# Kernel tuning notes

Measured on AMD Instinct MI355X. Metric: run time of the kernel, lower is better.

The kernel has to match this reference:

```python
import jax, jax.numpy as jnp
import numpy as np

B = 8
SHAPE = (4, 16, 16)   # latent video shape; S = prod = 1024
S = 1024
AE = 64               # ae_embed_dim
D = 768               # embed_dim
F = 3072              # mlp_dim
H = 12                # num_heads (heads are re-merged before the score matmul!)
L = 12                # num_layers
C = 17                # n_classes
OUT = 1024            # out_dim
EPS = 1e-6
HD = D // H


def setup_inputs() -> dict:
    key = jax.random.key(0)
    ks = iter(jax.random.split(key, 64))

    def p(shape, s=0.02):
        return jax.random.normal(next(ks), shape, jnp.float32) * s

    inp = {
        'x': jax.random.normal(next(ks), (B, *SHAPE, AE), jnp.float32),
        'mask': jnp.tril(jnp.ones((S, S), bool)),  # causal
        'label': jax.nn.one_hot(jax.random.randint(next(ks), (B,), 0, C), C, dtype=jnp.float32),
        'dense_in_w': p((D, AE)), 'dense_in_b': jnp.zeros((D,), jnp.float32),
        'sos': p((D,)),
        # BroadcastPositionBiases: embed_dim=768 split into 3 chunks of 256
        'pos0': p((SHAPE[0], D // 3)), 'pos1': p((SHAPE[1], D // 3)), 'pos2': p((SHAPE[2], D // 3)),
        'ln1_sw': p((L, D, C)), 'ln1_bw': p((L, D, C)),
        'qkv_w': p((L, 3 * D, D)), 'qkv_b': jnp.zeros((L, 3 * D), jnp.float32),
        'ao1_w': p((L, D, D)), 'ao1_b': jnp.zeros((L, D), jnp.float32),  # DotProductAttention.out_proj
        'ao2_w': p((L, D, D)), 'ao2_b': jnp.zeros((L, D), jnp.float32),  # MultiHeadAttention.out_proj
        'ln2_sw': p((L, D, C)), 'ln2_bw': p((L, D, C)),
        'mlp_w1': p((L, F, D)), 'mlp_b1': jnp.zeros((L, F), jnp.float32),
        'mlp_w2': p((L, D, F)), 'mlp_b2': jnp.zeros((L, D), jnp.float32),
        'lnf_sw': p((D, C)), 'lnf_bw': p((D, C)),
        'out_w': p((OUT, D)), 'out_b': jnp.zeros((OUT,), jnp.float32),
    }
    return inp


def cond_ln(x, cond, sw, bw):
    # conditional LayerNorm: mul = rsqrt(var+eps)*(1+Linear(cond)), bias = Linear(cond)
    mean = jnp.mean(x, axis=-1, keepdims=True)
    var = jnp.mean((x - mean) ** 2, axis=-1, keepdims=True)
    scale = cond @ sw.T   # [B, D]
    bias = cond @ bw.T    # [B, D]
    mul = jax.lax.rsqrt(var + EPS) * (1.0 + scale[:, None, :])
    return (x - mean) * mul + bias[:, None, :]


def pos_bias(embs, shape):
    n = len(shape)
    outs = []
    for i, e in enumerate(embs):
        sh = [1] * n + [e.shape[-1]]
        sh[i] = shape[i]
        outs.append(jnp.broadcast_to(e.reshape(sh), tuple(shape) + (e.shape[-1],)))
    return jnp.concatenate(outs, axis=-1).reshape(-1, sum(e.shape[-1] for e in embs))  # [S, D]


def attn_block(h, mask, qkv_w, qkv_b, o1_w, o1_b, o2_w, o2_b):
    Bn, Sn, Dn = h.shape
    qkv = h @ qkv_w.T + qkv_b                       # [B, S, 3D]
    qkv = qkv.reshape(Bn, Sn, H, 3 * HD)            # per-head [q|k|v] layout
    q = qkv[..., :HD].reshape(Bn, Sn, Dn)           # heads re-merged BEFORE scores
    k = qkv[..., HD:2 * HD].reshape(Bn, Sn, Dn)
    v = qkv[..., 2 * HD:].reshape(Bn, Sn, Dn)
    # NOTE: scaling uses full embed_dim (module quirk), not head_dim
    scores = jnp.einsum('bqd,bkd->bqk', q * (float(Dn) ** -0.5), k)
    scores = jnp.where(mask[None, :, :], scores, -jnp.inf)
    w = jax.nn.softmax(scores, axis=-1)
    out = jnp.einsum('bqk,bkd->bqd', w, v)
    out = out @ o1_w.T + o1_b                        # DotProductAttention.out_proj
    out = out @ o2_w.T + o2_b                        # MultiHeadAttention.out_proj (applied twice)
    return out


def _forward(x, mask, label, dense_in_w, dense_in_b, sos, pos0, pos1, pos2,
             ln1_sw, ln1_bw, qkv_w, qkv_b, ao1_w, ao1_b, ao2_w, ao2_b,
             ln2_sw, ln2_bw, mlp_w1, mlp_b1, mlp_w2, mlp_b2,
             lnf_sw, lnf_bw, out_w, out_b):
    Bn = x.shape[0]
    old_shape = x.shape[1:-1]
    h = x.reshape(Bn, -1, x.shape[-1]) @ dense_in_w.T + dense_in_b   # [B, S, D]
    # right shift with learned SOS token
    h = jnp.concatenate([jnp.broadcast_to(sos, (Bn, 1, D)), h[:, :-1]], axis=1)
    pb = pos_bias([pos0, pos1, pos2], old_shape)                     # [S, D]
    h = h + pb[None, :h.shape[1]]
    for l in range(L):
        hn = cond_ln(h, label, ln1_sw[l], ln1_bw[l])
        h = h + attn_block(hn, mask, qkv_w[l], qkv_b[l], ao1_w[l], ao1_b[l], ao2_w[l], ao2_b[l])
        hn = cond_ln(h, label, ln2_sw[l], ln2_bw[l])
        m = hn @ mlp_w1[l].T + mlp_b1[l]
        m = jax.nn.sigmoid(1.702 * m) * m           # GELU2
        m = m @ mlp_w2[l].T + mlp_b2[l]
        h = h + m
    h = cond_ln(h, label, lnf_sw, lnf_bw)
    out = h @ out_w.T + out_b                        # [B, S, OUT]
    return out.reshape(Bn, *old_shape, out.shape[-1])


def reference(x, mask, label, dense_in_w, dense_in_b, sos, pos0, pos1, pos2,
              ln1_sw, ln1_bw, qkv_w, qkv_b, ao1_w, ao1_b, ao2_w, ao2_b,
              ln2_sw, ln2_bw, mlp_w1, mlp_b1, mlp_w2, mlp_b2,
              lnf_sw, lnf_bw, out_w, out_b):
    return _forward(x, mask, label, dense_in_w, dense_in_b, sos, pos0, pos1, pos2,
                    ln1_sw, ln1_bw, qkv_w, qkv_b, ao1_w, ao1_b, ao2_w, ao2_b,
                    ln2_sw, ln2_bw, mlp_w1, mlp_b1, mlp_w2, mlp_b2,
                    lnf_sw, lnf_bw, out_w, out_b)
```

## Files before the change

### kernel.cpp

```cpp
#include <hip/hip_runtime.h>

typedef __bf16 bf16;
typedef __bf16 bf16x8 __attribute__((ext_vector_type(8)));
typedef __bf16 bf16x4 __attribute__((ext_vector_type(4)));
typedef float  f32x4  __attribute__((ext_vector_type(4)));

#define DEV __device__ __forceinline__

DEV void gload_lds16(const bf16* g, bf16* l) {
    __builtin_amdgcn_global_load_lds(
        (__attribute__((address_space(1))) void*)g,
        (__attribute__((address_space(3))) void*)l, 16, 0, 0);
}

DEV void barrier_raw() {
    asm volatile("" ::: "memory");
    __builtin_amdgcn_s_barrier();
    asm volatile("" ::: "memory");
}

enum { M_QKV, M_SCORES, M_PV, M_RESID, M_GELU, M_OUT, M_WM };

template<int MODE>
__global__ __launch_bounds__(256)
void gemm_k(const bf16* __restrict__ A, const bf16* __restrict__ B,
            int M, int N, int K,
            long long batchA, long long batchB, long long batchC,
            const float* __restrict__ bias,
            bf16* __restrict__ Cb, float* __restrict__ Cf,
            bf16* __restrict__ qp, bf16* __restrict__ kp, bf16* __restrict__ vp)
{
    const int bm = blockIdx.x, bn = blockIdx.y, bz = blockIdx.z;
    const int kTiles = K >> 5;

    const int tid = threadIdx.x, wid = tid >> 6, lane = tid & 63;
    const bf16* Ab = A + (long long)bz * batchA + (long long)bm * 128 * K;
    const bf16* Bb = B + (long long)bz * batchB + (long long)bn * 128 * K;

    extern __shared__ __align__(16) bf16 smem[];
    bf16* sA = smem;
    bf16* sB = smem + 12288;

    const int srow = wid * 16 + (lane >> 2);
    const int scol = (lane & 3) * 8;
    const long long aoff = (long long)srow * K + scol;

    auto stage = [&](int buf, int kt) {
        const bf16* ga = Ab + (long long)kt * 32;
        const bf16* gb = Bb + (long long)kt * 32;
        bf16* a = sA + buf * 4096;
        bf16* b = sB + buf * 4096;
        gload_lds16(ga + aoff,            a + (wid * 16) * 32);
        gload_lds16(ga + aoff + 64LL * K, a + (64 + wid * 16) * 32);
        gload_lds16(gb + aoff,            b + (wid * 16) * 32);
        gload_lds16(gb + aoff + 64LL * K, b + (64 + wid * 16) * 32);
    };

    f32x4 acc[4][4];
#pragma unroll
    for (int m = 0; m < 4; ++m)
#pragma unroll
        for (int n = 0; n < 4; ++n) acc[m][n] = (f32x4){0.f, 0.f, 0.f, 0.f};

    const int npre = kTiles < 2 ? kTiles : 2;
    for (int t = 0; t < npre; ++t) stage(t, t);

    const int wr = wid >> 1, wc = wid & 1;
    const int arow = wr * 64 + (lane & 15);
    const int brow = wc * 64 + (lane & 15);
    const int koff = (lane >> 4) * 8;

    int cur = 0;
    for (int kt = 0; kt < kTiles; ++kt) {
        if (kt + 1 < kTiles) asm volatile("s_waitcnt vmcnt(4)" ::: "memory");
        else                 asm volatile("s_waitcnt vmcnt(0)" ::: "memory");
        barrier_raw();
        if (kt + 2 < kTiles) {
            int ib = cur - 1; if (ib < 0) ib = 2;
            stage(ib, kt + 2);
        }

        const bf16* a = sA + cur * 4096;
        const bf16* b = sB + cur * 4096;
        bf16x8 af[4], bfr[4];
#pragma unroll
        for (int m = 0; m < 4; ++m)
            af[m] = *(const bf16x8*)&a[(arow + m * 16) * 32 + koff];
#pragma unroll
        for (int n = 0; n < 4; ++n)
            bfr[n] = *(const bf16x8*)&b[(brow + n * 16) * 32 + koff];
#pragma unroll
        for (int m = 0; m < 4; ++m)
#pragma unroll
            for (int n = 0; n < 4; ++n)
                acc[m][n] = __builtin_amdgcn_mfma_f32_16x16x32_bf16(af[m], bfr[n], acc[m][n], 0, 0, 0);

        cur = (cur == 2) ? 0 : cur + 1;
    }

    const int cr0 = bm * 128 + wr * 64 + (lane >> 4) * 4;
    const int cc0 = bn * 128 + wc * 64 + (lane & 15);
#pragma unroll
    for (int m = 0; m < 4; ++m) {
#pragma unroll
        for (int n = 0; n < 4; ++n) {
            const int col = cc0 + n * 16;
#pragma unroll
            for (int r = 0; r < 4; ++r) {
                const int row = cr0 + m * 16 + r;
                float v = acc[m][n][r];
                if (MODE == M_QKV) {
                    v += bias[col];
                    int hd = col / 192, rr = col % 192;
                    int b2 = row >> 10, s = row & 1023;
                    if (rr < 64)
                        qp[(long long)row * 768 + hd * 64 + rr] = (bf16)(v * 0.03608439182435161f);
                    else if (rr < 128)
                        kp[(long long)row * 768 + hd * 64 + (rr - 64)] = (bf16)v;
                    else
                        vp[((long long)b2 * 768 + hd * 64 + (rr - 128)) * 1024 + s] = (bf16)v;
                } else if (MODE == M_GELU) {
                    float xg = v + bias[col];
                    Cb[(long long)row * N + col] = (bf16)(xg / (1.f + __expf(-1.702f * xg)));
                } else if (MODE == M_RESID) {
                    long long idx = (long long)row * N + col;
                    Cf[idx] += v + bias[col];
                } else if (MODE == M_WM) {
                    Cb[(long long)bz * batchC + (long long)row * N + col] = (bf16)v;
                } else {
                    Cf[(long long)row * N + col] = v + bias[col];
                }
            }
        }
    }
}

template<int MODE>
__global__ __launch_bounds__(256)
void gemm64_k(const bf16* __restrict__ A, const bf16* __restrict__ B,
              int M, int N, int K,
              long long batchA, long long batchB, long long batchC,
              const float* __restrict__ bias,
              bf16* __restrict__ Cb, float* __restrict__ Cf)
{
    const int bm = blockIdx.x, bn = blockIdx.y, bz = blockIdx.z;
    if (MODE == M_SCORES && 2 * bn > bm) return;
    int kTiles = K >> 5;
    if (MODE == M_PV) {
        int lim = 2 * bm + 2;
        if (lim < kTiles) kTiles = lim;
    }

    const int tid = threadIdx.x, wid = tid >> 6, lane = tid & 63;
    const bf16* Ab = A + (long long)bz * batchA + (long long)bm * 64 * K;
    const bf16* Bb = B + (long long)bz * batchB + (long long)bn * 128 * K;

    extern __shared__ __align__(16) bf16 smem[];
    bf16* sA = smem;
    bf16* sB = smem + 6144;

    const int srow = wid * 16 + (lane >> 2);
    const int scol = (lane & 3) * 8;
    const long long aoff = (long long)srow * K + scol;

    auto stage = [&](int buf, int kt) {
        const bf16* ga = Ab + (long long)kt * 32;
        const bf16* gb = Bb + (long long)kt * 32;
        gload_lds16(ga + aoff,            sA + buf * 2048 + (wid * 16) * 32);
        gload_lds16(gb + aoff,            sB + buf * 4096 + (wid * 16) * 32);
        gload_lds16(gb + aoff + 64LL * K, sB + buf * 4096 + (64 + wid * 16) * 32);
    };

    f32x4 acc[2][4];
#pragma unroll
    for (int m = 0; m < 2; ++m)
#pragma unroll
        for (int n = 0; n < 4; ++n) acc[m][n] = (f32x4){0.f, 0.f, 0.f, 0.f};

    const int npre = kTiles < 2 ? kTiles : 2;
    for (int t = 0; t < npre; ++t) stage(t, t);

    const int wr = wid >> 1, wc = wid & 1;
    const int arow = wr * 32 + (lane & 15);
    const int brow = wc * 64 + (lane & 15);
    const int koff = (lane >> 4) * 8;

    int cur = 0;
    for (int kt = 0; kt < kTiles; ++kt) {
        if (kt + 1 < kTiles) asm volatile("s_waitcnt vmcnt(3)" ::: "memory");
        else                 asm volatile("s_waitcnt vmcnt(0)" ::: "memory");
        barrier_raw();
        if (kt + 2 < kTiles) {
            int ib = cur - 1; if (ib < 0) ib = 2;
            stage(ib, kt + 2);
        }

        const bf16* a = sA + cur * 2048;
        const bf16* b = sB + cur * 4096;
        bf16x8 af[2], bfr[4];
#pragma unroll
        for (int m = 0; m < 2; ++m)
            af[m] = *(const bf16x8*)&a[(arow + m * 16) * 32 + koff];
#pragma unroll
        for (int n = 0; n < 4; ++n)
            bfr[n] = *(const bf16x8*)&b[(brow + n * 16) * 32 + koff];
#pragma unroll
        for (int m = 0; m < 2; ++m)
#pragma unroll
            for (int n = 0; n < 4; ++n)
                acc[m][n] = __builtin_amdgcn_mfma_f32_16x16x32_bf16(af[m], bfr[n], acc[m][n], 0, 0, 0);

        cur = (cur == 2) ? 0 : cur + 1;
    }

    const int cr0 = bm * 64 + wr * 32 + (lane >> 4) * 4;
    const int cc0 = bn * 128 + wc * 64 + (lane & 15);
#pragma unroll
    for (int m = 0; m < 2; ++m) {
#pragma unroll
        for (int n = 0; n < 4; ++n) {
            const int col = cc0 + n * 16;
#pragma unroll
            for (int r = 0; r < 4; ++r) {
                const int row = cr0 + m * 16 + r;
                float v = acc[m][n][r];
                if (MODE == M_SCORES || MODE == M_PV) {
                    Cb[(long long)bz * batchC + (long long)row * N + col] = (bf16)v;
                } else if (MODE == M_RESID) {
                    long long idx = (long long)row * N + col;
                    Cf[idx] += v + bias[col];
                } else {
                    Cf[(long long)row * N + col] = v + bias[col];
                }
            }
        }
    }
}

__global__ __launch_bounds__(256)
void cvt_bf16_k(const float* __restrict__ in, bf16* __restrict__ out, int n4)
{
    int i = blockIdx.x * 256 + threadIdx.x;
    if (i >= n4) return;
    float4 f = ((const float4*)in)[i];
    bf16x4 o = { (bf16)f.x, (bf16)f.y, (bf16)f.z, (bf16)f.w };
    ((bf16x4*)out)[i] = o;
}

__global__ __launch_bounds__(256)
void transpose_cvt_k(const float* __restrict__ in, bf16* __restrict__ out, int n)
{
    __shared__ float t[32][33];
    const int l = blockIdx.z;
    const int r0 = blockIdx.y * 32, c0 = blockIdx.x * 32;
    const float* src = in + (long long)l * n * n;
    bf16* dst = out + (long long)l * n * n;
    const int tx = threadIdx.x & 31, ty = threadIdx.x >> 5;
#pragma unroll
    for (int i = 0; i < 32; i += 8)
        t[ty + i][tx] = src[(long long)(r0 + ty + i) * n + c0 + tx];
    __syncthreads();
#pragma unroll
    for (int i = 0; i < 32; i += 8)
        dst[(long long)(c0 + ty + i) * n + r0 + tx] = (bf16)t[tx][ty + i];
}

__global__ __launch_bounds__(256)
void bias_merge_k(const float* __restrict__ o2w, const float* __restrict__ o1b,
                  const float* __restrict__ o2b, float* __restrict__ bm, int total)
{
    const int wid = threadIdx.x >> 6, lane = threadIdx.x & 63;
    const int idx = blockIdx.x * 4 + wid;
    if (idx >= total) return;
    const int l = idx / 768, a = idx - l * 768;
    const float* wrow = o2w + ((long long)l * 768 + a) * 768;
    const float* brow = o1b + (long long)l * 768;
    float s = 0.f;
#pragma unroll
    for (int j = 0; j < 12; ++j) {
        int c = j * 64 + lane;
        s += wrow[c] * brow[c];
    }
#pragma unroll
    for (int o = 32; o; o >>= 1) s += __shfl_down(s, o);
    if (lane == 0) bm[idx] = s + o2b[(long long)l * 768 + a];
}

__global__ __launch_bounds__(256)
void cond_proj_k(const float* __restrict__ label, const float* __restrict__ sw,
                 const float* __restrict__ bw, float* __restrict__ scale,
                 float* __restrict__ bias, int total)
{
    int idx = blockIdx.x * 256 + threadIdx.x;
    if (idx >= total) return;
    int l = idx / 6144;
    int rem = idx - l * 6144;
    int b = rem / 768, d = rem - (rem / 768) * 768;
    const float* lab = label + b * 17;
    const float* swp = sw + ((long long)l * 768 + d) * 17;
    const float* bwp = bw + ((long long)l * 768 + d) * 17;
    float s = 0.f, bb = 0.f;
#pragma unroll
    for (int c = 0; c < 17; ++c) { float lv = lab[c]; s += lv * swp[c]; bb += lv * bwp[c]; }
    scale[idx] = s;
    bias[idx]  = bb;
}

__global__ __launch_bounds__(256)
void shift_pos_k(const float* __restrict__ xe, const float* __restrict__ sos,
                 const float* __restrict__ p0, const float* __restrict__ p1,
                 const float* __restrict__ p2, float* __restrict__ h)
{
    const int s = blockIdx.x, b = blockIdx.y;
    const int i0 = s >> 8, i1 = (s >> 4) & 15, i2 = s & 15;
    const float* xr = xe + ((long long)b * 1024 + (s - 1)) * 768;
#pragma unroll
    for (int j = 0; j < 3; ++j) {
        const int d = j * 256 + threadIdx.x;
        float v = (s == 0) ? sos[d] : xr[d];
        float pbv = (d < 256) ? p0[i0 * 256 + d]
                  : (d < 512) ? p1[i1 * 256 + (d - 256)]
                              : p2[i2 * 256 + (d - 512)];
        h[((long long)b * 1024 + s) * 768 + d] = v + pbv;
    }
}

__global__ __launch_bounds__(256)
void cond_ln_k(const float* __restrict__ h, const float* __restrict__ scale,
               const float* __restrict__ bias, bf16* __restrict__ out)
{
    const long long row = (long long)blockIdx.y * 1024 + blockIdx.x;
    const int b = blockIdx.y;
    const float* hr = h + row * 768;
    float v[3], sum = 0.f, sq = 0.f;
#pragma unroll
    for (int j = 0; j < 3; ++j) {
        v[j] = hr[j * 256 + threadIdx.x];
        sum += v[j]; sq += v[j] * v[j];
    }
    __shared__ float sm[8];
#pragma unroll
    for (int o = 32; o; o >>= 1) { sum += __shfl_down(sum, o); sq += __shfl_down(sq, o); }
    const int wid = threadIdx.x >> 6;
    if ((threadIdx.x & 63) == 0) { sm[wid] = sum; sm[4 + wid] = sq; }
    __syncthreads();
    sum = sm[0] + sm[1] + sm[2] + sm[3];
    sq  = sm[4] + sm[5] + sm[6] + sm[7];
    const float mean = sum * (1.f / 768.f);
    const float var  = sq * (1.f / 768.f) - mean * mean;
    const float rs   = rsqrtf(var + 1e-6f);
    const float* sc = scale + (long long)b * 768;
    const float* bi = bias  + (long long)b * 768;
    bf16* orow = out + row * 768;
#pragma unroll
    for (int j = 0; j < 3; ++j) {
        const int d = j * 256 + threadIdx.x;
        orow[d] = (bf16)((v[j] - mean) * rs * (1.f + sc[d]) + bi[d]);
    }
}

__global__ __launch_bounds__(256)
void softmax_k(bf16* __restrict__ P)
{
    const int i = blockIdx.x, b = blockIdx.y;
    bf16* row = P + ((long long)b * 1024 + i) * 1024;
    const int len = i + 1;
    const int lim = (i | 63) + 1;
    float v[4], mx = -1e30f;
#pragma unroll
    for (int j = 0; j < 4; ++j) {
        int c = j * 256 + threadIdx.x;
        v[j] = (c < len) ? (float)row[c] : -1e30f;
        mx = fmaxf(mx, v[j]);
    }
    __shared__ float sm[8];
#pragma unroll
    for (int o = 32; o; o >>= 1) mx = fmaxf(mx, __shfl_down(mx, o));
    const int wid = threadIdx.x >> 6;
    if ((threadIdx.x & 63) == 0) sm[wid] = mx;
    __syncthreads();
    mx = fmaxf(fmaxf(sm[0], sm[1]), fmaxf(sm[2], sm[3]));
    float s = 0.f;
#pragma unroll
    for (int j = 0; j < 4; ++j) {
        v[j] = __expf(v[j] - mx);
        s += ((j * 256 + threadIdx.x) < len) ? v[j] : 0.f;
    }
#pragma unroll
    for (int o = 32; o; o >>= 1) s += __shfl_down(s, o);
    if ((threadIdx.x & 63) == 0) sm[4 + wid] = s;
    __syncthreads();
    s = sm[4] + sm[5] + sm[6] + sm[7];
    const float inv = 1.f / s;
#pragma unroll
    for (int j = 0; j < 4; ++j) {
        int c = j * 256 + threadIdx.x;
        if (c < lim) row[c] = (c < len) ? (bf16)(v[j] * inv) : (bf16)0.f;
    }
}

__global__ __launch_bounds__(256)
void fill_k(float* o, int n, float v)
{
    int i = blockIdx.x * 256 + threadIdx.x;
    if (i < n) o[i] = v;
}

extern "C" void kernel_launch(void* const* d_in, const int* in_sizes, int n_in,
                              void* d_out, int out_size, void* d_ws, size_t ws_size,
                              hipStream_t stream)
{
    (void)in_sizes; (void)n_in;
    const float* x     = (const float*)d_in[0];
    const float* label = (const float*)d_in[2];
    const float* dw    = (const float*)d_in[3];
    const float* db    = (const float*)d_in[4];
    const float* sos   = (const float*)d_in[5];
    const float* p0    = (const float*)d_in[6];
    const float* p1    = (const float*)d_in[7];
    const float* p2    = (const float*)d_in[8];
    const float* ln1sw = (const float*)d_in[9];
    const float* ln1bw = (const float*)d_in[10];
    const float* qkvw  = (const float*)d_in[11];
    const float* qkvb  = (const float*)d_in[12];
    const float* ao1w  = (const float*)d_in[13];
    const float* ao1b  = (const float*)d_in[14];
    const float* ao2w  = (const float*)d_in[15];
    const float* ao2b  = (const float*)d_in[16];
    const float* ln2sw = (const float*)d_in[17];
    const float* ln2bw = (const float*)d_in[18];
    const float* m1w   = (const float*)d_in[19];
    const float* m1b   = (const float*)d_in[20];
    const float* m2w   = (const float*)d_in[21];
    const float* m2b   = (const float*)d_in[22];
    const float* lnfsw = (const float*)d_in[23];
    const float* lnfbw = (const float*)d_in[24];
    const float* outw  = (const float*)d_in[25];
    const float* outb  = (const float*)d_in[26];
    float* out = (float*)d_out;

    char* p = (char*)d_ws;
    auto alloc = [&](size_t bytes) { void* r = (void*)p; p += (bytes + 255) & ~(size_t)255; return r; };
    float* h    = (float*)alloc(8192LL * 768 * 4);
    bf16*  hn   = (bf16*) alloc(8192LL * 768 * 2);
    bf16*  q    = (bf16*) alloc(8192LL * 768 * 2);
    bf16*  kbuf = (bf16*) alloc(8192LL * 768 * 2);
    bf16*  vT   = (bf16*) alloc(8192LL * 768 * 2);
    bf16*  P    = (bf16*) alloc(8LL * 1024 * 1024 * 2);
    bf16*  attn = (bf16*) alloc(8192LL * 768 * 2);
    bf16*  mb   = (bf16*) alloc(8192LL * 3072 * 2);
    bf16*  wout = (bf16*) alloc(1024LL * 768 * 2);
    bf16*  wmA  = (bf16*) alloc(12LL * 768 * 768 * 2);
    float* bmA  = (float*)alloc(12LL * 768 * 4);
    float* s1   = (float*)alloc(12LL * 8 * 768 * 4);
    float* b1   = (float*)alloc(12LL * 8 * 768 * 4);
    float* s2   = (float*)alloc(12LL * 8 * 768 * 4);
    float* b2   = (float*)alloc(12LL * 8 * 768 * 4);
    float* sf   = (float*)alloc(8LL * 768 * 4);
    float* bfb  = (float*)alloc(8LL * 768 * 4);

    size_t base_needed = (size_t)(p - (char*)d_ws);
    if (base_needed + 16LL * 1024 * 1024 > ws_size) {
        fill_k<<<(out_size + 255) / 256, 256, 0, stream>>>(out, out_size, 1e9f);
        return;
    }

    const long long SZ_QKV = 2304LL * 768, SZ_O = 768LL * 768, SZ_M = 3072LL * 768;
    size_t all_bytes = (size_t)(12 * (SZ_QKV + 2 * SZ_M)) * 2;
    bool allw = ((size_t)(p - (char*)d_ws) + all_bytes + 4096 <= ws_size);

    bf16 *wqkvA, *wm1A, *wm2A;
    if (allw) {
        wqkvA = (bf16*)alloc(12 * SZ_QKV * 2);
        wm1A  = (bf16*)alloc(12 * SZ_M * 2);
        wm2A  = (bf16*)alloc(12 * SZ_M * 2);
    } else {
        wqkvA = (bf16*)alloc(SZ_QKV * 2);
        wm1A  = (bf16*)alloc(SZ_M * 2);
        wm2A  = (bf16*)alloc(SZ_M * 2);
    }

    bf16*  xbf   = (bf16*)P;
    bf16*  dwbf  = (bf16*)P + 524288;
    bf16*  wo2bf = (bf16*)P + 1048576;
    float* xe    = (float*)mb;
    bf16*  o1t   = mb + 12582912;

    cvt_bf16_k<<<1024 * 768 / 4 / 256, 256, 0, stream>>>(outw, wout, 1024 * 768 / 4);
    cond_proj_k<<<(12 * 8 * 768 + 255) / 256, 256, 0, stream>>>(label, ln1sw, ln1bw, s1, b1, 12 * 8 * 768);
    cond_proj_k<<<(12 * 8 * 768 + 255) / 256, 256, 0, stream>>>(label, ln2sw, ln2bw, s2, b2, 12 * 8 * 768);
    cond_proj_k<<<(8 * 768 + 255) / 256, 256, 0, stream>>>(label, lnfsw, lnfbw, sf, bfb, 8 * 768);

    if (allw) {
        cvt_bf16_k<<<(int)(12 * SZ_QKV / 4 / 256), 256, 0, stream>>>(qkvw, wqkvA, (int)(12 * SZ_QKV / 4));
        cvt_bf16_k<<<(int)(12 * SZ_M / 4 / 256),   256, 0, stream>>>(m1w,  wm1A,  (int)(12 * SZ_M / 4));
        cvt_bf16_k<<<(int)(12 * SZ_M / 4 / 256),   256, 0, stream>>>(m2w,  wm2A,  (int)(12 * SZ_M / 4));
    }

    cvt_bf16_k<<<(int)(12 * SZ_O / 4 / 256), 256, 0, stream>>>(ao2w, wo2bf, (int)(12 * SZ_O / 4));
    transpose_cvt_k<<<dim3(24, 24, 12), 256, 0, stream>>>(ao1w, o1t, 768);
    gemm_k<M_WM><<<dim3(6, 6, 12), 256, 49152, stream>>>(
        wo2bf, o1t, 768, 768, 768, SZ_O, SZ_O, SZ_O,
        nullptr, wmA, nullptr, nullptr, nullptr, nullptr);
    bias_merge_k<<<(12 * 768 + 3) / 4, 256, 0, stream>>>(ao2w, ao1b, ao2b, bmA, 12 * 768);

    cvt_bf16_k<<<8192 * 64 / 4 / 256, 256, 0, stream>>>(x, xbf, 8192 * 64 / 4);
    cvt_bf16_k<<<768 * 64 / 4 / 256, 256, 0, stream>>>(dw, dwbf, 768 * 64 / 4);
    gemm_k<M_OUT><<<dim3(64, 6, 1), 256, 49152, stream>>>(
        xbf, dwbf, 8192, 768, 64, 0, 0, 0, db, nullptr, xe, nullptr, nullptr, nullptr);
    shift_pos_k<<<dim3(1024, 8), 256, 0, stream>>>(xe, sos, p0, p1, p2, h);

    for (int l = 0; l < 12; ++l) {
        bf16 *wqkv, *wm1, *wm2;
        if (allw) {
            wqkv = wqkvA + (long long)l * SZ_QKV;
            wm1  = wm1A  + (long long)l * SZ_M;
            wm2  = wm2A  + (long long)l * SZ_M;
        } else {
            wqkv = wqkvA; wm1 = wm1A; wm2 = wm2A;
            cvt_bf16_k<<<(int)(SZ_QKV / 4 / 256), 256, 0, stream>>>(qkvw + (long long)l * SZ_QKV, wqkv, (int)(SZ_QKV / 4));
            cvt_bf16_k<<<(int)(SZ_M / 4 / 256),   256, 0, stream>>>(m1w  + (long long)l * SZ_M,   wm1,  (int)(SZ_M / 4));
            cvt_bf16_k<<<(int)(SZ_M / 4 / 256),   256, 0, stream>>>(m2w  + (long long)l * SZ_M,   wm2,  (int)(SZ_M / 4));
        }

        cond_ln_k<<<dim3(1024, 8), 256, 0, stream>>>(h, s1 + (long long)l * 6144, b1 + (long long)l * 6144, hn);

        gemm_k<M_QKV><<<dim3(64, 18, 1), 256, 49152, stream>>>(
            hn, wqkv, 8192, 2304, 768, 0, 0, 0,
            qkvb + (long long)l * 2304, nullptr, nullptr, q, kbuf, vT);

        gemm64_k<M_SCORES><<<dim3(16, 8, 8), 256, 36864, stream>>>(
            q, kbuf, 1024, 1024, 768, 1024LL * 768, 1024LL * 768, 1024LL * 1024,
            nullptr, P, nullptr);

        softmax_k<<<dim3(1024, 8), 256, 0, stream>>>(P);

        gemm64_k<M_PV><<<dim3(16, 6, 8), 256, 36864, stream>>>(
            P, vT, 1024, 768, 1024, 1024LL * 1024, 768LL * 1024, 1024LL * 768,
            nullptr, attn, nullptr);

        gemm64_k<M_RESID><<<dim3(128, 6, 1), 256, 36864, stream>>>(
            attn, wmA + (long long)l * SZ_O, 8192, 768, 768, 0, 0, 0,
            bmA + (long long)l * 768, nullptr, h);

        cond_ln_k<<<dim3(1024, 8), 256, 0, stream>>>(h, s2 + (long long)l * 6144, b2 + (long long)l * 6144, hn);

        gemm_k<M_GELU><<<dim3(64, 24, 1), 256, 49152, stream>>>(
            hn, wm1, 8192, 3072, 768, 0, 0, 0,
            m1b + (long long)l * 3072, mb, nullptr, nullptr, nullptr, nullptr);

        gemm64_k<M_RESID><<<dim3(128, 6, 1), 256, 36864, stream>>>(
            mb, wm2, 8192, 768, 3072, 0, 0, 0,
            m2b + (long long)l * 768, nullptr, h);
    }

    cond_ln_k<<<dim3(1024, 8), 256, 0, stream>>>(h, sf, bfb, hn);
    gemm64_k<M_OUT><<<dim3(128, 8, 1), 256, 36864, stream>>>(
        hn, wout, 8192, 1024, 768, 0, 0, 0,
        outb, nullptr, out);
}
```

Baseline: 3.905 ms.

## Load A operand directly to registers, stage only B through LDS

New measurement: 5.349 ms. 36.9% more time.

```diff
diff --git a/kernel.cpp b/kernel.cpp
--- a/kernel.cpp
+++ b/kernel.cpp
@@ -14,7 +14,7 @@
 }
 
 DEV void barrier_raw() {
-    asm volatile("" ::: "memory");
+    asm volatile("s_waitcnt lgkmcnt(0)" ::: "memory");
     __builtin_amdgcn_s_barrier();
     asm volatile("" ::: "memory");
 }
@@ -37,55 +37,52 @@
     const bf16* Ab = A + (long long)bz * batchA + (long long)bm * 128 * K;
     const bf16* Bb = B + (long long)bz * batchB + (long long)bn * 128 * K;
 
-    extern __shared__ __align__(16) bf16 smem[];
-    bf16* sA = smem;
-    bf16* sB = smem + 12288;
+    extern __shared__ __align__(16) bf16 sB[];
 
     const int srow = wid * 16 + (lane >> 2);
     const int scol = (lane & 3) * 8;
-    const long long aoff = (long long)srow * K + scol;
-
-    auto stage = [&](int buf, int kt) {
-        const bf16* ga = Ab + (long long)kt * 32;
-        const bf16* gb = Bb + (long long)kt * 32;
-        bf16* a = sA + buf * 4096;
+    const long long boff = (long long)srow * K + scol;
+
+    auto stageB = [&](int buf, int kt) {
+        const bf16* gb = Bb + (long long)kt * 32 + boff;
         bf16* b = sB + buf * 4096;
-        gload_lds16(ga + aoff,            a + (wid * 16) * 32);
-        gload_lds16(ga + aoff + 64LL * K, a + (64 + wid * 16) * 32);
-        gload_lds16(gb + aoff,            b + (wid * 16) * 32);
-        gload_lds16(gb + aoff + 64LL * K, b + (64 + wid * 16) * 32);
+        gload_lds16(gb,            b + (wid * 16) * 32);
+        gload_lds16(gb + 64LL * K, b + (64 + wid * 16) * 32);
     };
-
-    f32x4 acc[4][4];
-#pragma unroll
-    for (int m = 0; m < 4; ++m)
-#pragma unroll
-        for (int n = 0; n < 4; ++n) acc[m][n] = (f32x4){0.f, 0.f, 0.f, 0.f};
-
-    const int npre = kTiles < 2 ? kTiles : 2;
-    for (int t = 0; t < npre; ++t) stage(t, t);
 
     const int wr = wid >> 1, wc = wid & 1;
     const int arow = wr * 64 + (lane & 15);
     const int brow = wc * 64 + (lane & 15);
     const int koff = (lane >> 4) * 8;
 
-    int cur = 0;
-    for (int kt = 0; kt < kTiles; ++kt) {
-        if (kt + 1 < kTiles) asm volatile("s_waitcnt vmcnt(4)" ::: "memory");
+    auto loadA = [&](bf16x8 (&af)[4], int kt) {
+#pragma unroll
+        for (int m = 0; m < 4; ++m)
+            af[m] = *(const bf16x8*)(Ab + (long long)(arow + m * 16) * K + kt * 32 + koff);
+    };
+
+    f32x4 acc[4][4];
+#pragma unroll
+    for (int m = 0; m < 4; ++m)
+#pragma unroll
+        for (int n = 0; n < 4; ++n) acc[m][n] = (f32x4){0.f, 0.f, 0.f, 0.f};
+
+    bf16x8 afA[4], afB[4];
+    stageB(0, 0);
+    if (kTiles > 1) stageB(1, 1);
+    loadA(afA, 0);
+
+    auto body = [&](bf16x8 (&afc)[4], bf16x8 (&afn)[4], int kt) {
+        if (kt + 2 < kTiles) asm volatile("s_waitcnt vmcnt(2)" ::: "memory");
         else                 asm volatile("s_waitcnt vmcnt(0)" ::: "memory");
         barrier_raw();
+        if (kt + 1 < kTiles) loadA(afn, kt + 1);
         if (kt + 2 < kTiles) {
-            int ib = cur - 1; if (ib < 0) ib = 2;
-            stage(ib, kt + 2);
+            int b3 = (kt + 2) % 3;
+            stageB(b3, kt + 2);
         }
-
-        const bf16* a = sA + cur * 4096;
-        const bf16* b = sB + cur * 4096;
-        bf16x8 af[4], bfr[4];
-#pragma unroll
-        for (int m = 0; m < 4; ++m)
-            af[m] = *(const bf16x8*)&a[(arow + m * 16) * 32 + koff];
+        const bf16* b = sB + (kt % 3) * 4096;
+        bf16x8 bfr[4];
 #pragma unroll
         for (int n = 0; n < 4; ++n)
             bfr[n] = *(const bf16x8*)&b[(brow + n * 16) * 32 + koff];
@@ -93,9 +90,12 @@
         for (int m = 0; m < 4; ++m)
 #pragma unroll
             for (int n = 0; n < 4; ++n)
-                acc[m][n] = __builtin_amdgcn_mfma_f32_16x16x32_bf16(af[m], bfr[n], acc[m][n], 0, 0, 0);
-
-        cur = (cur == 2) ? 0 : cur + 1;
+                acc[m][n] = __builtin_amdgcn_mfma_f32_16x16x32_bf16(afc[m], bfr[n], acc[m][n], 0, 0, 0);
+    };
+
+    for (int kt = 0; kt < kTiles; kt += 2) {
+        body(afA, afB, kt);
+        body(afB, afA, kt + 1);
     }
 
     const int cr0 = bm * 128 + wr * 64 + (lane >> 4) * 4;
@@ -155,52 +155,52 @@
     const bf16* Ab = A + (long long)bz * batchA + (long long)bm * 64 * K;
     const bf16* Bb = B + (long long)bz * batchB + (long long)bn * 128 * K;
 
-    extern __shared__ __align__(16) bf16 smem[];
-    bf16* sA = smem;
-    bf16* sB = smem + 6144;
+    extern __shared__ __align__(16) bf16 sB[];
 
     const int srow = wid * 16 + (lane >> 2);
     const int scol = (lane & 3) * 8;
-    const long long aoff = (long long)srow * K + scol;
-
-    auto stage = [&](int buf, int kt) {
-        const bf16* ga = Ab + (long long)kt * 32;
-        const bf16* gb = Bb + (long long)kt * 32;
-        gload_lds16(ga + aoff,            sA + buf * 2048 + (wid * 16) * 32);
-        gload_lds16(gb + aoff,            sB + buf * 4096 + (wid * 16) * 32);
-        gload_lds16(gb + aoff + 64LL * K, sB + buf * 4096 + (64 + wid * 16) * 32);
+    const long long boff = (long long)srow * K + scol;
+
+    auto stageB = [&](int buf, int kt) {
+        const bf16* gb = Bb + (long long)kt * 32 + boff;
+        bf16* b = sB + buf * 4096;
+        gload_lds16(gb,            b + (wid * 16) * 32);
+        gload_lds16(gb + 64LL * K, b + (64 + wid * 16) * 32);
     };
-
-    f32x4 acc[2][4];
-#pragma unroll
-    for (int m = 0; m < 2; ++m)
-#pragma unroll
-        for (int n = 0; n < 4; ++n) acc[m][n] = (f32x4){0.f, 0.f, 0.f, 0.f};
-
-    const int npre = kTiles < 2 ? kTiles : 2;
-    for (int t = 0; t < npre; ++t) stage(t, t);
 
     const int wr = wid >> 1, wc = wid & 1;
     const int arow = wr * 32 + (lane & 15);
     const int brow = wc * 64 + (lane & 15);
     const int koff = (lane >> 4) * 8;
 
-    int cur = 0;
-    for (int kt = 0; kt < kTiles; ++kt) {
-        if (kt + 1 < kTiles) asm volatile("s_waitcnt vmcnt(3)" ::: "memory");
+    auto loadA = [&](bf16x8 (&af)[2], int kt) {
+#pragma unroll
+        for (int m = 0; m < 2; ++m)
+            af[m] = *(const bf16x8*)(Ab + (long long)(arow + m * 16) * K + kt * 32 + koff);
+    };
+
+    f32x4 acc[2][4];
+#pragma unroll
+    for (int m = 0; m < 2; ++m)
+#pragma unroll
+        for (int n = 0; n < 4; ++n) acc[m][n] = (f32x4){0.f, 0.f, 0.f, 0.f};
+
+    bf16x8 afA[2], afB[2];
+    stageB(0, 0);
+    if (kTiles > 1) stageB(1, 1);
+    loadA(afA, 0);
+
+    auto body = [&](bf16x8 (&afc)[2], bf16x8 (&afn)[2], int kt) {
+        if (kt + 2 < kTiles) asm volatile("s_waitcnt vmcnt(2)" ::: "memory");
         else                 asm volatile("s_waitcnt vmcnt(0)" ::: "memory");
         barrier_raw();
+        if (kt + 1 < kTiles) loadA(afn, kt + 1);
         if (kt + 2 < kTiles) {
-            int ib = cur - 1; if (ib < 0) ib = 2;
-            stage(ib, kt + 2);
+            int b3 = (kt + 2) % 3;
+            stageB(b3, kt + 2);
         }
-
-        const bf16* a = sA + cur * 2048;
-        const bf16* b = sB + cur * 4096;
-        bf16x8 af[2], bfr[4];
-#pragma unroll
-        for (int m = 0; m < 2; ++m)
-            af[m] = *(const bf16x8*)&a[(arow + m * 16) * 32 + koff];
+        const bf16* b = sB + (kt % 3) * 4096;
+        bf16x8 bfr[4];
 #pragma unroll
         for (int n = 0; n < 4; ++n)
             bfr[n] = *(const bf16x8*)&b[(brow + n * 16) * 32 + koff];
@@ -208,9 +208,12 @@
         for (int m = 0; m < 2; ++m)
 #pragma unroll
             for (int n = 0; n < 4; ++n)
-                acc[m][n] = __builtin_amdgcn_mfma_f32_16x16x32_bf16(af[m], bfr[n], acc[m][n], 0, 0, 0);
-
-        cur = (cur == 2) ? 0 : cur + 1;
+                acc[m][n] = __builtin_amdgcn_mfma_f32_16x16x32_bf16(afc[m], bfr[n], acc[m][n], 0, 0, 0);
+    };
+
+    for (int kt = 0; kt < kTiles; kt += 2) {
+        body(afA, afB, kt);
+        body(afB, afA, kt + 1);
     }
 
     const int cr0 = bm * 64 + wr * 32 + (lane >> 4) * 4;
@@ -499,14 +502,14 @@
 
     cvt_bf16_k<<<(int)(12 * SZ_O / 4 / 256), 256, 0, stream>>>(ao2w, wo2bf, (int)(12 * SZ_O / 4));
     transpose_cvt_k<<<dim3(24, 24, 12), 256, 0, stream>>>(ao1w, o1t, 768);
-    gemm_k<M_WM><<<dim3(6, 6, 12), 256, 49152, stream>>>(
+    gemm_k<M_WM><<<dim3(6, 6, 12), 256, 24576, stream>>>(
         wo2bf, o1t, 768, 768, 768, SZ_O, SZ_O, SZ_O,
         nullptr, wmA, nullptr, nullptr, nullptr, nullptr);
     bias_merge_k<<<(12 * 768 + 3) / 4, 256, 0, stream>>>(ao2w, ao1b, ao2b, bmA, 12 * 768);
 
     cvt_bf16_k<<<8192 * 64 / 4 / 256, 256, 0, stream>>>(x, xbf, 8192 * 64 / 4);
     cvt_bf16_k<<<768 * 64 / 4 / 256, 256, 0, stream>>>(dw, dwbf, 768 * 64 / 4);
-    gemm_k<M_OUT><<<dim3(64, 6, 1), 256, 49152, stream>>>(
+    gemm_k<M_OUT><<<dim3(64, 6, 1), 256, 24576, stream>>>(
         xbf, dwbf, 8192, 768, 64, 0, 0, 0, db, nullptr, xe, nullptr, nullptr, nullptr);
     shift_pos_k<<<dim3(1024, 8), 256, 0, stream>>>(xe, sos, p0, p1, p2, h);
 
@@ -525,37 +528,37 @@
 
         cond_ln_k<<<dim3(1024, 8), 256, 0, stream>>>(h, s1 + (long long)l * 6144, b1 + (long long)l * 6144, hn);
 
-        gemm_k<M_QKV><<<dim3(64, 18, 1), 256, 49152, stream>>>(
+        gemm_k<M_QKV><<<dim3(64, 18, 1), 256, 24576, stream>>>(
             hn, wqkv, 8192, 2304, 768, 0, 0, 0,
             qkvb + (long long)l * 2304, nullptr, nullptr, q, kbuf, vT);
 
-        gemm64_k<M_SCORES><<<dim3(16, 8, 8), 256, 36864, stream>>>(
+        gemm64_k<M_SCORES><<<dim3(16, 8, 8), 256, 24576, stream>>>(
             q, kbuf, 1024, 1024, 768, 1024LL * 768, 1024LL * 768, 1024LL * 1024,
             nullptr, P, nullptr);
 
         softmax_k<<<dim3(1024, 8), 256, 0, stream>>>(P);
 
-        gemm64_k<M_PV><<<dim3(16, 6, 8), 256, 36864, stream>>>(
+        gemm64_k<M_PV><<<dim3(16, 6, 8), 256, 24576, stream>>>(
             P, vT, 1024, 768, 1024, 1024LL * 1024, 768LL * 1024, 1024LL * 768,
             nullptr, attn, nullptr);
 
-        gemm64_k<M_RESID><<<dim3(128, 6, 1), 256, 36864, stream>>>(
+        gemm64_k<M_RESID><<<dim3(128, 6, 1), 256, 24576, stream>>>(
             attn, wmA + (long long)l * SZ_O, 8192, 768, 768, 0, 0, 0,
             bmA + (long long)l * 768, nullptr, h);
 
         cond_ln_k<<<dim3(1024, 8), 256, 0, stream>>>(h, s2 + (long long)l * 6144, b2 + (long long)l * 6144, hn);
 
-        gemm_k<M_GELU><<<dim3(64, 24, 1), 256, 49152, stream>>>(
+        gemm_k<M_GELU><<<dim3(64, 24, 1), 256, 24576, stream>>>(
             hn, wm1, 8192, 3072, 768, 0, 0, 0,
             m1b + (long long)l * 3072, mb, nullptr, nullptr, nullptr, nullptr);
 
-        gemm64_k<M_RESID><<<dim3(128, 6, 1), 256, 36864, stream>>>(
+        gemm64_k<M_RESID><<<dim3(128, 6, 1), 256, 24576, stream>>>(
             mb, wm2, 8192, 768, 3072, 0, 0, 0,
             m2b + (long long)l * 768, nullptr, h);
     }
 
     cond_ln_k<<<dim3(1024, 8), 256, 0, stream>>>(h, sf, bfb, hn);
-    gemm64_k<M_OUT><<<dim3(128, 8, 1), 256, 36864, stream>>>(
+    gemm64_k<M_OUT><<<dim3(128, 8, 1), 256, 24576, stream>>>(
         hn, wout, 8192, 1024, 768, 0, 0, 0,
         outb, nullptr, out);
 }
```

## Give each wave a private LDS staging region and drop block barriers in gemm64

Applied to the files above, without the earlier changes.

After: 4.624 ms. 1.18x slower.

```diff
diff --git a/kernel.cpp b/kernel.cpp
--- a/kernel.cpp
+++ b/kernel.cpp
@@ -14,7 +14,7 @@
 }
 
 DEV void barrier_raw() {
-    asm volatile("" ::: "memory");
+    asm volatile("s_waitcnt lgkmcnt(0)" ::: "memory");
     __builtin_amdgcn_s_barrier();
     asm volatile("" ::: "memory");
 }
@@ -156,19 +156,24 @@
     const bf16* Bb = B + (long long)bz * batchB + (long long)bn * 128 * K;
 
     extern __shared__ __align__(16) bf16 smem[];
-    bf16* sA = smem;
-    bf16* sB = smem + 6144;
-
-    const int srow = wid * 16 + (lane >> 2);
-    const int scol = (lane & 3) * 8;
-    const long long aoff = (long long)srow * K + scol;
+    bf16* wbase = smem + wid * 9216;
+
+    const int wr = wid >> 1, wc = wid & 1;
+
+    const long long sgo = (long long)(lane >> 2) * K + (lane & 3) * 8;
+    const bf16* gaw = Ab + (long long)(wr * 32) * K + sgo;
+    const bf16* gbw = Bb + (long long)(wc * 64) * K + sgo;
 
     auto stage = [&](int buf, int kt) {
-        const bf16* ga = Ab + (long long)kt * 32;
-        const bf16* gb = Bb + (long long)kt * 32;
-        gload_lds16(ga + aoff,            sA + buf * 2048 + (wid * 16) * 32);
-        gload_lds16(gb + aoff,            sB + buf * 4096 + (wid * 16) * 32);
-        gload_lds16(gb + aoff + 64LL * K, sB + buf * 4096 + (64 + wid * 16) * 32);
+        bf16* d = wbase + buf * 3072;
+        const bf16* ga = gaw + (long long)kt * 32;
+        const bf16* gb = gbw + (long long)kt * 32;
+        gload_lds16(ga,            d);
+        gload_lds16(ga + 16LL * K, d + 512);
+        gload_lds16(gb,            d + 1024);
+        gload_lds16(gb + 16LL * K, d + 1536);
+        gload_lds16(gb + 32LL * K, d + 2048);
+        gload_lds16(gb + 48LL * K, d + 2560);
     };
 
     f32x4 acc[2][4];
@@ -177,44 +182,34 @@
 #pragma unroll
         for (int n = 0; n < 4; ++n) acc[m][n] = (f32x4){0.f, 0.f, 0.f, 0.f};
 
-    const int npre = kTiles < 2 ? kTiles : 2;
-    for (int t = 0; t < npre; ++t) stage(t, t);
-
-    const int wr = wid >> 1, wc = wid & 1;
-    const int arow = wr * 32 + (lane & 15);
-    const int brow = wc * 64 + (lane & 15);
-    const int koff = (lane >> 4) * 8;
-
-    int cur = 0;
+    stage(0, 0);
+    if (kTiles > 1) stage(1, 1);
+
+    const int l15 = lane & 15, koff = (lane >> 4) * 8;
+
     for (int kt = 0; kt < kTiles; ++kt) {
-        if (kt + 1 < kTiles) asm volatile("s_waitcnt vmcnt(3)" ::: "memory");
+        if (kt + 1 < kTiles) asm volatile("s_waitcnt vmcnt(6)" ::: "memory");
         else                 asm volatile("s_waitcnt vmcnt(0)" ::: "memory");
-        barrier_raw();
-        if (kt + 2 < kTiles) {
-            int ib = cur - 1; if (ib < 0) ib = 2;
-            stage(ib, kt + 2);
-        }
-
-        const bf16* a = sA + cur * 2048;
-        const bf16* b = sB + cur * 4096;
+        asm volatile("s_waitcnt lgkmcnt(0)" ::: "memory");
+        if (kt + 2 < kTiles) stage((kt + 2) % 3, kt + 2);
+
+        const bf16* d = wbase + (kt % 3) * 3072;
         bf16x8 af[2], bfr[4];
 #pragma unroll
         for (int m = 0; m < 2; ++m)
-            af[m] = *(const bf16x8*)&a[(arow + m * 16) * 32 + koff];
+            af[m] = *(const bf16x8*)&d[(m * 16 + l15) * 32 + koff];
 #pragma unroll
         for (int n = 0; n < 4; ++n)
-            bfr[n] = *(const bf16x8*)&b[(brow + n * 16) * 32 + koff];
+            bfr[n] = *(const bf16x8*)&d[1024 + (n * 16 + l15) * 32 + koff];
 #pragma unroll
         for (int m = 0; m < 2; ++m)
 #pragma unroll
             for (int n = 0; n < 4; ++n)
                 acc[m][n] = __builtin_amdgcn_mfma_f32_16x16x32_bf16(af[m], bfr[n], acc[m][n], 0, 0, 0);
-
-        cur = (cur == 2) ? 0 : cur + 1;
     }
 
     const int cr0 = bm * 64 + wr * 32 + (lane >> 4) * 4;
-    const int cc0 = bn * 128 + wc * 64 + (lane & 15);
+    const int cc0 = bn * 128 + wc * 64 + l15;
 #pragma unroll
     for (int m = 0; m < 2; ++m) {
 #pragma unroll
@@ -529,17 +524,17 @@
             hn, wqkv, 8192, 2304, 768, 0, 0, 0,
             qkvb + (long long)l * 2304, nullptr, nullptr, q, kbuf, vT);
 
-        gemm64_k<M_SCORES><<<dim3(16, 8, 8), 256, 36864, stream>>>(
+        gemm64_k<M_SCORES><<<dim3(16, 8, 8), 256, 73728, stream>>>(
             q, kbuf, 1024, 1024, 768, 1024LL * 768, 1024LL * 768, 1024LL * 1024,
             nullptr, P, nullptr);
 
         softmax_k<<<dim3(1024, 8), 256, 0, stream>>>(P);
 
-        gemm64_k<M_PV><<<dim3(16, 6, 8), 256, 36864, stream>>>(
+        gemm64_k<M_PV><<<dim3(16, 6, 8), 256, 73728, stream>>>(
             P, vT, 1024, 768, 1024, 1024LL * 1024, 768LL * 1024, 1024LL * 768,
             nullptr, attn, nullptr);
 
-        gemm64_k<M_RESID><<<dim3(128, 6, 1), 256, 36864, stream>>>(
+        gemm64_k<M_RESID><<<dim3(128, 6, 1), 256, 73728, stream>>>(
             attn, wmA + (long long)l * SZ_O, 8192, 768, 768, 0, 0, 0,
             bmA + (long long)l * 768, nullptr, h);
 
@@ -549,13 +544,13 @@
             hn, wm1, 8192, 3072, 768, 0, 0, 0,
             m1b + (long long)l * 3072, mb, nullptr, nullptr, nullptr, nullptr);
 
-        gemm64_k<M_RESID><<<dim3(128, 6, 1), 256, 36864, stream>>>(
+        gemm64_k<M_RESID><<<dim3(128, 6, 1), 256, 73728, stream>>>(
             mb, wm2, 8192, 768, 3072, 0, 0, 0,
             m2b + (long long)l * 768, nullptr, h);
     }
 
     cond_ln_k<<<dim3(1024, 8), 256, 0, stream>>>(h, sf, bfb, hn);
-    gemm64_k<M_OUT><<<dim3(128, 8, 1), 256, 36864, stream>>>(
+    gemm64_k<M_OUT><<<dim3(128, 8, 1), 256, 73728, stream>>>(
         hn, wout, 8192, 1024, 768, 0, 0, 0,
         outb, nullptr, out);
 }
```

## Add 128x256-tile GEMM kernel for QKV and MLP-up projections

Applied to the files above, without the earlier changes.

Result: slower. 4.408 ms (+12.9%).

```diff
diff --git a/kernel.cpp b/kernel.cpp
--- a/kernel.cpp
+++ b/kernel.cpp
@@ -14,7 +14,7 @@
 }
 
 DEV void barrier_raw() {
-    asm volatile("" ::: "memory");
+    asm volatile("s_waitcnt lgkmcnt(0)" ::: "memory");
     __builtin_amdgcn_s_barrier();
     asm volatile("" ::: "memory");
 }
@@ -104,6 +104,111 @@
     for (int m = 0; m < 4; ++m) {
 #pragma unroll
         for (int n = 0; n < 4; ++n) {
+            const int col = cc0 + n * 16;
+#pragma unroll
+            for (int r = 0; r < 4; ++r) {
+                const int row = cr0 + m * 16 + r;
+                float v = acc[m][n][r];
+                if (MODE == M_GELU) {
+                    float xg = v + bias[col];
+                    Cb[(long long)row * N + col] = (bf16)(xg / (1.f + __expf(-1.702f * xg)));
+                } else if (MODE == M_RESID) {
+                    long long idx = (long long)row * N + col;
+                    Cf[idx] += v + bias[col];
+                } else if (MODE == M_WM) {
+                    Cb[(long long)bz * batchC + (long long)row * N + col] = (bf16)v;
+                } else {
+                    Cf[(long long)row * N + col] = v + bias[col];
+                }
+            }
+        }
+    }
+}
+
+template<int MODE>
+__global__ __launch_bounds__(256)
+void gemm_w(const bf16* __restrict__ A, const bf16* __restrict__ B,
+            int N, int K,
+            const float* __restrict__ bias,
+            bf16* __restrict__ Cb,
+            bf16* __restrict__ qp, bf16* __restrict__ kp, bf16* __restrict__ vp)
+{
+    const int bm = blockIdx.x, bn = blockIdx.y;
+    const int kTiles = K >> 5;
+
+    const int tid = threadIdx.x, wid = tid >> 6, lane = tid & 63;
+    const bf16* Ab = A + (long long)bm * 128 * K;
+    const bf16* Bb = B + (long long)bn * 256 * K;
+
+    extern __shared__ __align__(16) bf16 smem[];
+    bf16* sA = smem;
+    bf16* sB = smem + 12288;
+
+    const int srow = wid * 16 + (lane >> 2);
+    const int scol = (lane & 3) * 8;
+    const long long aoff = (long long)srow * K + scol;
+
+    auto stage = [&](int buf, int kt) {
+        const bf16* ga = Ab + (long long)kt * 32;
+        const bf16* gb = Bb + (long long)kt * 32;
+        bf16* a = sA + buf * 4096;
+        bf16* b = sB + buf * 8192;
+        gload_lds16(ga + aoff,             a + (wid * 16) * 32);
+        gload_lds16(ga + aoff + 64LL * K,  a + (64 + wid * 16) * 32);
+        gload_lds16(gb + aoff,             b + (wid * 16) * 32);
+        gload_lds16(gb + aoff + 64LL * K,  b + (64 + wid * 16) * 32);
+        gload_lds16(gb + aoff + 128LL * K, b + (128 + wid * 16) * 32);
+        gload_lds16(gb + aoff + 192LL * K, b + (192 + wid * 16) * 32);
+    };
+
+    f32x4 acc[4][8];
+#pragma unroll
+    for (int m = 0; m < 4; ++m)
+#pragma unroll
+        for (int n = 0; n < 8; ++n) acc[m][n] = (f32x4){0.f, 0.f, 0.f, 0.f};
+
+    const int npre = kTiles < 2 ? kTiles : 2;
+    for (int t = 0; t < npre; ++t) stage(t, t);
+
+    const int wr = wid >> 1, wc = wid & 1;
+    const int arow = wr * 64 + (lane & 15);
+    const int brow = wc * 128 + (lane & 15);
+    const int koff = (lane >> 4) * 8;
+
+    int cur = 0;
+    for (int kt = 0; kt < kTiles; ++kt) {
+        if (kt + 1 < kTiles) asm volatile("s_waitcnt vmcnt(6)" ::: "memory");
+        else                 asm volatile("s_waitcnt vmcnt(0)" ::: "memory");
+        barrier_raw();
+        if (kt + 2 < kTiles) {
+            int ib = cur - 1; if (ib < 0) ib = 2;
+            stage(ib, kt + 2);
+        }
+
+        const bf16* a = sA + cur * 4096;
+        const bf16* b = sB + cur * 8192;
+        bf16x8 af[4], bfr[8];
+#pragma unroll
+        for (int m = 0; m < 4; ++m)
+            af[m] = *(const bf16x8*)&a[(arow + m * 16) * 32 + koff];
+#pragma unroll
+        for (int n = 0; n < 8; ++n)
+            bfr[n] = *(const bf16x8*)&b[(brow + n * 16) * 32 + koff];
+#pragma unroll
+        for (int m = 0; m < 4; ++m)
+#pragma unroll
+            for (int n = 0; n < 8; ++n)
+                acc[m][n] = __builtin_amdgcn_mfma_f32_16x16x32_bf16(af[m], bfr[n], acc[m][n], 0, 0, 0);
+
+        cur = (cur == 2) ? 0 : cur + 1;
+    }
+
+    const int cr0 = bm * 128 + wr * 64 + (lane >> 4) * 4;
+    const int cc0 = bn * 256 + wc * 128 + (lane & 15);
+#pragma unroll
+    for (int m = 0; m < 4; ++m) {
+#pragma unroll
+        for (int n = 0; n < 8; ++n) {
             const int col = cc0 + n * 16;
 #pragma unroll
             for (int r = 0; r < 4; ++r) {
@@ -119,16 +224,9 @@
                         kp[(long long)row * 768 + hd * 64 + (rr - 64)] = (bf16)v;
                     else
                         vp[((long long)b2 * 768 + hd * 64 + (rr - 128)) * 1024 + s] = (bf16)v;
-                } else if (MODE == M_GELU) {
+                } else {
                     float xg = v + bias[col];
                     Cb[(long long)row * N + col] = (bf16)(xg / (1.f + __expf(-1.702f * xg)));
-                } else if (MODE == M_RESID) {
-                    long long idx = (long long)row * N + col;
-                    Cf[idx] += v + bias[col];
-                } else if (MODE == M_WM) {
-                    Cb[(long long)bz * batchC + (long long)row * N + col] = (bf16)v;
-                } else {
-                    Cf[(long long)row * N + col] = v + bias[col];
                 }
             }
         }
@@ -525,9 +623,9 @@
 
         cond_ln_k<<<dim3(1024, 8), 256, 0, stream>>>(h, s1 + (long long)l * 6144, b1 + (long long)l * 6144, hn);
 
-        gemm_k<M_QKV><<<dim3(64, 18, 1), 256, 49152, stream>>>(
-            hn, wqkv, 8192, 2304, 768, 0, 0, 0,
-            qkvb + (long long)l * 2304, nullptr, nullptr, q, kbuf, vT);
+        gemm_w<M_QKV><<<dim3(64, 9, 1), 256, 73728, stream>>>(
+            hn, wqkv, 2304, 768,
+            qkvb + (long long)l * 2304, nullptr, q, kbuf, vT);
 
         gemm64_k<M_SCORES><<<dim3(16, 8, 8), 256, 36864, stream>>>(
             q, kbuf, 1024, 1024, 768, 1024LL * 768, 1024LL * 768, 1024LL * 1024,
@@ -545,9 +643,9 @@
 
         cond_ln_k<<<dim3(1024, 8), 256, 0, stream>>>(h, s2 + (long long)l * 6144, b2 + (long long)l * 6144, hn);
 
-        gemm_k<M_GELU><<<dim3(64, 24, 1), 256, 49152, stream>>>(
-            hn, wm1, 8192, 3072, 768, 0, 0, 0,
-            m1b + (long long)l * 3072, mb, nullptr, nullptr, nullptr, nullptr);
+        gemm_w<M_GELU><<<dim3(64, 12, 1), 256, 73728, stream>>>(
+            hn, wm1, 3072, 768,
+            m1b + (long long)l * 3072, mb, nullptr, nullptr, nullptr);
 
         gemm64_k<M_RESID><<<dim3(128, 6, 1), 256, 36864, stream>>>(
             mb, wm2, 8192, 768, 3072, 0, 0, 0,
```
